# Kernel optimization log

Hardware: AMD Instinct MI355X
Metric: run time of the kernel (lower is better)

Reference implementation:

```python
import jax, jax.numpy as jnp
import numpy as np

D_MODEL = 1024
D_ATTN = 1024
BATCH = 4
SEQ = 2048


def setup_inputs() -> dict:
    key = jax.random.key(0)
    k_x, k_q, k_k, k_v = jax.random.split(key, 4)
    return {
        "x": jax.random.normal(k_x, (BATCH, SEQ, D_MODEL), dtype=jnp.float32),
        "Wq": jax.random.normal(k_q, (D_MODEL, D_ATTN), dtype=jnp.float32),
        "Wk": jax.random.normal(k_k, (D_MODEL, D_ATTN), dtype=jnp.float32),
        "Wv": jax.random.normal(k_v, (D_MODEL, D_ATTN), dtype=jnp.float32),
    }


def reference(x, Wq, Wk, Wv):
    # x: [B, S, D]; Wq/Wk/Wv: [D, Da]
    B, S, _ = x.shape
    Da = Wq.shape[1]
    Q = jnp.einsum("bsd,da->bsa", x, Wq)
    K = jnp.einsum("bsd,da->bsa", x, Wk)
    V = jnp.einsum("bsd,da->bsa", x, Wv)
    scores = jnp.einsum("bia,bja->bij", Q, K)  # [B, S, S]
    # Faithful to source: tril with diagonal=1 (allows attending one step ahead)
    i = jnp.arange(S)[:, None]
    j = jnp.arange(S)[None, :]
    allowed = j <= i + 1  # [S, S] bool
    scores = jnp.where(allowed[None, :, :], scores, -jnp.inf)
    scale = jnp.sqrt(jnp.asarray(Da, dtype=scores.dtype))
    attn = jax.nn.softmax(scores / scale, axis=-1)
    # dropout p=0 -> identity
    return jnp.einsum("bij,bja->bia", attn, V)
```

## Files before the change

kernel.cpp:

```cpp
#include <hip/hip_runtime.h>
#include <math.h>

#define BATCH 4
#define SEQ 2048
#define DM 1024
#define NTOK (BATCH * SEQ)
#define NE ((size_t)NTOK * DM)
#define WN ((size_t)DM * DM)

using s16x8 = __attribute__((ext_vector_type(8))) short;
using f32x4 = __attribute__((ext_vector_type(4))) float;

__device__ __forceinline__ unsigned short f2bf(float f) {
    unsigned u = __builtin_bit_cast(unsigned, f);
    u += 0x7FFFu + ((u >> 16) & 1u);
    return (unsigned short)(u >> 16);
}
__device__ __forceinline__ float bf2f(unsigned short h) {
    unsigned u = ((unsigned)h) << 16;
    return __builtin_bit_cast(float, u);
}

__device__ __forceinline__ f32x4 MFMA(s16x8 a, s16x8 b, f32x4 c) {
    return __builtin_amdgcn_mfma_f32_16x16x32_bf16(a, b, c, 0, 0, 0);
}

#define AS1 __attribute__((address_space(1)))
#define AS3 __attribute__((address_space(3)))
__device__ __forceinline__ void gll16(const void* g, void* l) {
    __builtin_amdgcn_global_load_lds((const AS1 void*)g, (AS3 void*)l, 16, 0, 0);
}

__device__ __forceinline__ s16x8 lds_frag(const short* base, int row, int g) {
    return *(const s16x8*)(base + row * 64 + ((g ^ (row & 7)) << 3));
}

__device__ __forceinline__ void stage_tile(const unsigned short* g0, size_t rs,
                                           short* lds, int tid) {
    int lane = tid & 63, w = tid >> 6;
    #pragma unroll
    for (int c = 0; c < 4; ++c) {
        int s = c * 256 + w * 64 + lane;
        int row = s >> 3, gg = s & 7;
        int graw = gg ^ (row & 7);
        gll16(g0 + (size_t)row * rs + graw * 8, lds + (size_t)s * 8);
    }
}

__global__ __launch_bounds__(256) void split_x(const float* __restrict__ x,
                                               unsigned short* __restrict__ xh,
                                               unsigned short* __restrict__ xl) {
    size_t n4 = NE / 4;
    for (size_t i = (size_t)blockIdx.x * 256 + threadIdx.x; i < n4;
         i += (size_t)gridDim.x * 256) {
        float4 v = ((const float4*)x)[i];
        ushort4 h, l;
        h.x = f2bf(v.x); l.x = f2bf(v.x - bf2f(h.x));
        h.y = f2bf(v.y); l.y = f2bf(v.y - bf2f(h.y));
        h.z = f2bf(v.z); l.z = f2bf(v.z - bf2f(h.z));
        h.w = f2bf(v.w); l.w = f2bf(v.w - bf2f(h.w));
        ((ushort4*)xh)[i] = h;
        ((ushort4*)xl)[i] = l;
    }
}

__global__ __launch_bounds__(256) void split_w(
    const float* __restrict__ Wq, const float* __restrict__ Wk,
    const float* __restrict__ Wv,
    unsigned short* __restrict__ Wqh, unsigned short* __restrict__ Wql,
    unsigned short* __restrict__ Wkh, unsigned short* __restrict__ Wkl,
    unsigned short* __restrict__ Wvt) {
    const int z = blockIdx.z;
    const int tid = threadIdx.x;
    if (z < 2) {
        const float* W = z ? Wk : Wq;
        unsigned short* oh = z ? Wkh : Wqh;
        unsigned short* ol = z ? Wkl : Wql;
        size_t n4 = WN / 4;
        size_t stride = (size_t)gridDim.x * gridDim.y * 256;
        for (size_t i = ((size_t)blockIdx.y * gridDim.x + blockIdx.x) * 256 + tid;
             i < n4; i += stride) {
            float4 v = ((const float4*)W)[i];
            ushort4 h, l;
            h.x = f2bf(v.x); l.x = f2bf(v.x - bf2f(h.x));
            h.y = f2bf(v.y); l.y = f2bf(v.y - bf2f(h.y));
            h.z = f2bf(v.z); l.z = f2bf(v.z - bf2f(h.z));
            h.w = f2bf(v.w); l.w = f2bf(v.w - bf2f(h.w));
            ((ushort4*)oh)[i] = h;
            ((ushort4*)ol)[i] = l;
        }
    } else {
        __shared__ float t[64][65];
        const int d0 = blockIdx.x * 64, n0 = blockIdx.y * 64;
        #pragma unroll
        for (int c = 0; c < 16; ++c) {
            int f = c * 256 + tid; int r = f >> 6, cc = f & 63;
            t[r][cc] = Wv[(size_t)(d0 + r) * DM + n0 + cc];
        }
        __syncthreads();
        #pragma unroll
        for (int c = 0; c < 16; ++c) {
            int f = c * 256 + tid; int r = f >> 6, cc = f & 63;
            Wvt[(size_t)(n0 + r) * DM + d0 + cc] = f2bf(t[cc][r]);
        }
    }
}

__global__ __launch_bounds__(256, 2) void gemm3_split(
    const unsigned short* __restrict__ Ah_, const unsigned short* __restrict__ Al_,
    const unsigned short* __restrict__ Bh_, const unsigned short* __restrict__ Bl_,
    unsigned short* __restrict__ Ch, unsigned short* __restrict__ Cl) {
    const int m0 = blockIdx.x * 128, n0 = blockIdx.y * 128;
    __shared__ short Ah[128 * 64], Al[128 * 64], Bh[128 * 64], Bl[128 * 64];
    const int tid = threadIdx.x, lane = tid & 63, w = tid >> 6;
    const int wr = w >> 1, wc = w & 1;

    f32x4 acc[4][4];
    #pragma unroll
    for (int i = 0; i < 4; ++i)
        #pragma unroll
        for (int j = 0; j < 4; ++j) acc[i][j] = (f32x4){0.f, 0.f, 0.f, 0.f};

    for (int k0 = 0; k0 < DM; k0 += 64) {
        stage_tile(Ah_ + (size_t)m0 * DM + k0, DM, Ah, tid);
        stage_tile(Al_ + (size_t)m0 * DM + k0, DM, Al, tid);
        stage_tile(Bh_ + (size_t)n0 * DM + k0, DM, Bh, tid);
        stage_tile(Bl_ + (size_t)n0 * DM + k0, DM, Bl, tid);
        __syncthreads();
        #pragma unroll
        for (int ks = 0; ks < 2; ++ks) {
            const int g = ks * 4 + (lane >> 4);
            s16x8 a_h[4], a_l[4], b_h[4], b_l[4];
            #pragma unroll
            for (int mi = 0; mi < 4; ++mi) {
                int r = wr * 64 + mi * 16 + (lane & 15);
                a_h[mi] = lds_frag(Ah, r, g);
                a_l[mi] = lds_frag(Al, r, g);
            }
            #pragma unroll
            for (int ni = 0; ni < 4; ++ni) {
                int r = wc * 64 + ni * 16 + (lane & 15);
                b_h[ni] = lds_frag(Bh, r, g);
                b_l[ni] = lds_frag(Bl, r, g);
            }
            #pragma unroll
            for (int mi = 0; mi < 4; ++mi)
                #pragma unroll
                for (int ni = 0; ni < 4; ++ni) {
                    acc[mi][ni] = MFMA(a_h[mi], b_h[ni], acc[mi][ni]);
                    acc[mi][ni] = MFMA(a_h[mi], b_l[ni], acc[mi][ni]);
                    acc[mi][ni] = MFMA(a_l[mi], b_h[ni], acc[mi][ni]);
                }
        }
        __syncthreads();
    }
    #pragma unroll
    for (int mi = 0; mi < 4; ++mi)
        #pragma unroll
        for (int ni = 0; ni < 4; ++ni)
            #pragma unroll
            for (int r = 0; r < 4; ++r) {
                int row = m0 + wr * 64 + mi * 16 + (lane >> 4) * 4 + r;
                int col = n0 + wc * 64 + ni * 16 + (lane & 15);
                float v = acc[mi][ni][r];
                unsigned short h = f2bf(v);
                size_t o = (size_t)row * DM + col;
                Ch[o] = h;
                Cl[o] = f2bf(v - bf2f(h));
            }
}

__global__ __launch_bounds__(256, 2) void vt_mfma(
    const unsigned short* __restrict__ Wvt, const unsigned short* __restrict__ xh,
    unsigned short* __restrict__ Vt) {
    const int m0 = blockIdx.x * 128;
    const int n0 = blockIdx.y * 128;
    __shared__ short Ah[128 * 64], Bh[128 * 64];
    const int tid = threadIdx.x, lane = tid & 63, w = tid >> 6;
    const int wr = w >> 1, wc = w & 1;

    f32x4 acc[4][4];
    #pragma unroll
    for (int i = 0; i < 4; ++i)
        #pragma unroll
        for (int j = 0; j < 4; ++j) acc[i][j] = (f32x4){0.f, 0.f, 0.f, 0.f};

    for (int k0 = 0; k0 < DM; k0 += 64) {
        stage_tile(Wvt + (size_t)m0 * DM + k0, DM, Ah, tid);
        stage_tile(xh + (size_t)n0 * DM + k0, DM, Bh, tid);
        __syncthreads();
        #pragma unroll
        for (int ks = 0; ks < 2; ++ks) {
            const int g = ks * 4 + (lane >> 4);
            s16x8 a_h[4], b_h[4];
            #pragma unroll
            for (int mi = 0; mi < 4; ++mi)
                a_h[mi] = lds_frag(Ah, wr * 64 + mi * 16 + (lane & 15), g);
            #pragma unroll
            for (int ni = 0; ni < 4; ++ni)
                b_h[ni] = lds_frag(Bh, wc * 64 + ni * 16 + (lane & 15), g);
            #pragma unroll
            for (int mi = 0; mi < 4; ++mi)
                #pragma unroll
                for (int ni = 0; ni < 4; ++ni)
                    acc[mi][ni] = MFMA(a_h[mi], b_h[ni], acc[mi][ni]);
        }
        __syncthreads();
    }
    #pragma unroll
    for (int mi = 0; mi < 4; ++mi)
        #pragma unroll
        for (int ni = 0; ni < 4; ++ni)
            #pragma unroll
            for (int r = 0; r < 4; ++r) {
                int row = m0 + wr * 64 + mi * 16 + (lane >> 4) * 4 + r;
                int col = n0 + wc * 64 + ni * 16 + (lane & 15);
                Vt[(size_t)row * NTOK + col] = f2bf(acc[mi][ni][r]);
            }
}

__global__ __launch_bounds__(256, 2) void scores_mfma(
    const unsigned short* __restrict__ Yh, const unsigned short* __restrict__ Yl,
    const unsigned short* __restrict__ xh, const unsigned short* __restrict__ xl,
    float* __restrict__ P) {
    const int jt = blockIdx.x, t = blockIdx.y, b = blockIdx.z;
    if (jt > t + 1) return;
    const int m0 = t * 128, n0 = jt * 128;
    const size_t qrow0 = (size_t)b * SEQ + m0;
    const size_t krow0 = (size_t)b * SEQ + n0;

    __shared__ short Ah[128 * 64], Al[128 * 64], Bh[128 * 64], Bl[128 * 64];
    const int tid = threadIdx.x, lane = tid & 63, w = tid >> 6;
    const int wr = w >> 1, wc = w & 1;

    f32x4 acc[4][4];
    #pragma unroll
    for (int i = 0; i < 4; ++i)
        #pragma unroll
        for (int j = 0; j < 4; ++j) acc[i][j] = (f32x4){0.f, 0.f, 0.f, 0.f};

    for (int k0 = 0; k0 < DM; k0 += 64) {
        stage_tile(Yh + qrow0 * DM + k0, DM, Ah, tid);
        stage_tile(Yl + qrow0 * DM + k0, DM, Al, tid);
        stage_tile(xh + krow0 * DM + k0, DM, Bh, tid);
        stage_tile(xl + krow0 * DM + k0, DM, Bl, tid);
        __syncthreads();
        #pragma unroll
        for (int ks = 0; ks < 2; ++ks) {
            const int g = ks * 4 + (lane >> 4);
            s16x8 a_h[4], a_l[4], b_h[4], b_l[4];
            #pragma unroll
            for (int mi = 0; mi < 4; ++mi) {
                int r = wr * 64 + mi * 16 + (lane & 15);
                a_h[mi] = lds_frag(Ah, r, g);
                a_l[mi] = lds_frag(Al, r, g);
            }
            #pragma unroll
            for (int ni = 0; ni < 4; ++ni) {
                int r = wc * 64 + ni * 16 + (lane & 15);
                b_h[ni] = lds_frag(Bh, r, g);
                b_l[ni] = lds_frag(Bl, r, g);
            }
            #pragma unroll
            for (int mi = 0; mi < 4; ++mi)
                #pragma unroll
                for (int ni = 0; ni < 4; ++ni) {
                    acc[mi][ni] = MFMA(a_h[mi], b_h[ni], acc[mi][ni]);
                    acc[mi][ni] = MFMA(a_h[mi], b_l[ni], acc[mi][ni]);
                    acc[mi][ni] = MFMA(a_l[mi], b_h[ni], acc[mi][ni]);
                }
        }
        __syncthreads();
    }
    const float scale = 1.0f / 32.0f;
    #pragma unroll
    for (int mi = 0; mi < 4; ++mi)
        #pragma unroll
        for (int ni = 0; ni < 4; ++ni)
            #pragma unroll
            for (int r = 0; r < 4; ++r) {
                int i = m0 + wr * 64 + mi * 16 + (lane >> 4) * 4 + r;
                int j = n0 + wc * 64 + ni * 16 + (lane & 15);
                float v = (j <= i + 1) ? acc[mi][ni][r] * scale : -INFINITY;
                P[((size_t)b * SEQ + i) * SEQ + j] = v;
            }
}

__global__ __launch_bounds__(256) void softmax_bf16(
    const float* __restrict__ P, unsigned short* __restrict__ P2) {
    const int row = blockIdx.x;
    const int b = row >> 11, i = row & (SEQ - 1);
    const int t = i >> 7;
    const int L = min(SEQ, (t + 2) * 128);
    const float* p = P + ((size_t)b * SEQ + i) * SEQ;
    unsigned short* q = P2 + ((size_t)b * SEQ + i) * SEQ;
    const int tid = threadIdx.x;
    __shared__ float red[4];

    float v[8];
    #pragma unroll
    for (int c = 0; c < 8; ++c) {
        int j = c * 256 + tid;
        v[c] = (j < L) ? p[j] : -INFINITY;
    }
    float m = -INFINITY;
    #pragma unroll
    for (int c = 0; c < 8; ++c) m = fmaxf(m, v[c]);
    #pragma unroll
    for (int o = 32; o > 0; o >>= 1) m = fmaxf(m, __shfl_xor(m, o));
    if ((tid & 63) == 0) red[tid >> 6] = m;
    __syncthreads();
    m = fmaxf(fmaxf(red[0], red[1]), fmaxf(red[2], red[3]));
    __syncthreads();

    float s = 0.f;
    #pragma unroll
    for (int c = 0; c < 8; ++c) { v[c] = __expf(v[c] - m); s += v[c]; }
    #pragma unroll
    for (int o = 32; o > 0; o >>= 1) s += __shfl_xor(s, o);
    if ((tid & 63) == 0) red[tid >> 6] = s;
    __syncthreads();
    s = red[0] + red[1] + red[2] + red[3];
    const float inv = 1.f / s;

    #pragma unroll
    for (int c = 0; c < 8; ++c) {
        int j = c * 256 + tid;
        if (j < L) q[j] = f2bf(v[c] * inv);
    }
}

__global__ __launch_bounds__(256, 2) void pv_mfma(
    const unsigned short* __restrict__ P2, const unsigned short* __restrict__ Vt,
    float* __restrict__ Out) {
    const int bx = blockIdx.x, t = blockIdx.y, b = blockIdx.z;
    const int m0 = t * 128, n0 = bx * 128;
    const int jlim = min(SEQ, (t + 2) * 128);

    __shared__ short Pa[128 * 64], Vb[128 * 64];
    const int tid = threadIdx.x, lane = tid & 63, w = tid >> 6;
    const int wr = w >> 1, wc = w & 1;

    f32x4 acc[4][4];
    #pragma unroll
    for (int i = 0; i < 4; ++i)
        #pragma unroll
        for (int j = 0; j < 4; ++j) acc[i][j] = (f32x4){0.f, 0.f, 0.f, 0.f};

    for (int k0 = 0; k0 < jlim; k0 += 64) {
        stage_tile(P2 + ((size_t)b * SEQ + m0) * SEQ + k0, SEQ, Pa, tid);
        stage_tile(Vt + (size_t)n0 * NTOK + (size_t)b * SEQ + k0, NTOK, Vb, tid);
        __syncthreads();
        #pragma unroll
        for (int ks = 0; ks < 2; ++ks) {
            const int g = ks * 4 + (lane >> 4);
            s16x8 a_h[4], b_h[4];
            #pragma unroll
            for (int mi = 0; mi < 4; ++mi)
                a_h[mi] = lds_frag(Pa, wr * 64 + mi * 16 + (lane & 15), g);
            #pragma unroll
            for (int ni = 0; ni < 4; ++ni)
                b_h[ni] = lds_frag(Vb, wc * 64 + ni * 16 + (lane & 15), g);
            #pragma unroll
            for (int mi = 0; mi < 4; ++mi)
                #pragma unroll
                for (int ni = 0; ni < 4; ++ni)
                    acc[mi][ni] = MFMA(a_h[mi], b_h[ni], acc[mi][ni]);
        }
        __syncthreads();
    }
    #pragma unroll
    for (int mi = 0; mi < 4; ++mi)
        #pragma unroll
        for (int ni = 0; ni < 4; ++ni)
            #pragma unroll
            for (int r = 0; r < 4; ++r) {
                int i = m0 + wr * 64 + mi * 16 + (lane >> 4) * 4 + r;
                int col = n0 + wc * 64 + ni * 16 + (lane & 15);
                Out[((size_t)b * SEQ + i) * DM + col] = acc[mi][ni][r];
            }
}

extern "C" void kernel_launch(void* const* d_in, const int* in_sizes, int n_in,
                              void* d_out, int out_size, void* d_ws, size_t ws_size,
                              hipStream_t stream) {
    const float* x  = (const float*)d_in[0];
    const float* Wq = (const float*)d_in[1];
    const float* Wk = (const float*)d_in[2];
    const float* Wv = (const float*)d_in[3];

    char* ws = (char*)d_ws;
    unsigned short* Vt = (unsigned short*)ws;
    unsigned short* xh = (unsigned short*)(ws + 2 * NE);
    unsigned short* xl = (unsigned short*)(ws + 4 * NE);
    float* P = (float*)(ws + 6 * NE);
    unsigned short* P2 = (unsigned short*)(ws + 2 * NE);
    unsigned short* Wqh = (unsigned short*)(ws + 6 * NE);
    unsigned short* Wql = Wqh + WN;
    unsigned short* Wkh = Wql + WN;
    unsigned short* Wkl = Wkh + WN;
    unsigned short* Mh  = Wkl + WN;
    unsigned short* Ml  = Mh + WN;
    unsigned short* Wvt = Ml + WN;
    unsigned short* Yh = (unsigned short*)d_out;
    unsigned short* Yl = Yh + NE;

    split_x<<<2048, 256, 0, stream>>>(x, xh, xl);
    {
        dim3 g(16, 16, 3);
        split_w<<<g, 256, 0, stream>>>(Wq, Wk, Wv, Wqh, Wql, Wkh, Wkl, Wvt);
    }
    {
        dim3 g(8, 8);
        gemm3_split<<<g, 256, 0, stream>>>(Wkh, Wkl, Wqh, Wql, Mh, Ml);
    }
    {
        dim3 g(NTOK / 128, DM / 128);
        gemm3_split<<<g, 256, 0, stream>>>(xh, xl, Mh, Ml, Yh, Yl);
    }
    {
        dim3 g(DM / 128, NTOK / 128);
        vt_mfma<<<g, 256, 0, stream>>>(Wvt, xh, Vt);
    }
    {
        dim3 g(16, 16, 4);
        scores_mfma<<<g, 256, 0, stream>>>(Yh, Yl, xh, xl, P);
    }
    softmax_bf16<<<BATCH * SEQ, 256, 0, stream>>>(P, P2);
    {
        dim3 g(DM / 128, 16, 4);
        pv_mfma<<<g, 256, 0, stream>>>(P2, Vt, (float*)d_out);
    }
}
```

Baseline: 324.4 us.

## Split-K the Wk·Wqᵀ GEMM, fuse it with the V projection, and remap block order

The small 1024x1024 M = Wk·Wqᵀ GEMM, which previously launched only 64 blocks, is split 8-way along K into fp32 slabs. It runs in one fused launch alongside the V-projection blocks, and a separate reduce kernel sums the slabs and splits the result into bf16 hi/lo. Scores and PV kernels also remap linear block IDs so that consecutive blocks are strided across 8 groups, likely to spread work across XCDs and improve cache locality. The cost is extra fp32 slab traffic and one added launch.

```diff
diff --git a/kernel.cpp b/kernel.cpp
--- a/kernel.cpp
+++ b/kernel.cpp
@@ -106,6 +106,132 @@
     }
 }
 
+__global__ __launch_bounds__(256, 2) void mvt_fused(
+    const unsigned short* __restrict__ Wkh_, const unsigned short* __restrict__ Wkl_,
+    const unsigned short* __restrict__ Wqh_, const unsigned short* __restrict__ Wql_,
+    float* __restrict__ Mslab,
+    const unsigned short* __restrict__ Wvt_, const unsigned short* __restrict__ xh_,
+    unsigned short* __restrict__ Vt) {
+    __shared__ short L[4 * 128 * 64];
+    short* Ah = L;            short* Al = L + 128 * 64;
+    short* Bh = L + 2 * 128 * 64; short* Bl = L + 3 * 128 * 64;
+    const int tid = threadIdx.x, lane = tid & 63, w = tid >> 6;
+    const int wr = w >> 1, wc = w & 1;
+    const int bid = blockIdx.x;
+
+    f32x4 acc[4][4];
+    #pragma unroll
+    for (int i = 0; i < 4; ++i)
+        #pragma unroll
+        for (int j = 0; j < 4; ++j) acc[i][j] = (f32x4){0.f, 0.f, 0.f, 0.f};
+
+    if (bid < 512) {
+        const int kz = bid >> 6, rem = bid & 63;
+        const int m0 = (rem & 7) * 128, n0 = (rem >> 3) * 128;
+        #pragma unroll
+        for (int kk = 0; kk < 2; ++kk) {
+            const int k0 = kz * 128 + kk * 64;
+            stage_tile(Wkh_ + (size_t)m0 * DM + k0, DM, Ah, tid);
+            stage_tile(Wkl_ + (size_t)m0 * DM + k0, DM, Al, tid);
+            stage_tile(Wqh_ + (size_t)n0 * DM + k0, DM, Bh, tid);
+            stage_tile(Wql_ + (size_t)n0 * DM + k0, DM, Bl, tid);
+            __syncthreads();
+            #pragma unroll
+            for (int ks = 0; ks < 2; ++ks) {
+                const int g = ks * 4 + (lane >> 4);
+                s16x8 a_h[4], a_l[4], b_h[4], b_l[4];
+                #pragma unroll
+                for (int mi = 0; mi < 4; ++mi) {
+                    int r = wr * 64 + mi * 16 + (lane & 15);
+                    a_h[mi] = lds_frag(Ah, r, g);
+                    a_l[mi] = lds_frag(Al, r, g);
+                }
+                #pragma unroll
+                for (int ni = 0; ni < 4; ++ni) {
+                    int r = wc * 64 + ni * 16 + (lane & 15);
+                    b_h[ni] = lds_frag(Bh, r, g);
+                    b_l[ni] = lds_frag(Bl, r, g);
+                }
+                #pragma unroll
+                for (int mi = 0; mi < 4; ++mi)
+                    #pragma unroll
+                    for (int ni = 0; ni < 4; ++ni) {
+                        acc[mi][ni] = MFMA(a_h[mi], b_h[ni], acc[mi][ni]);
+                        acc[mi][ni] = MFMA(a_h[mi], b_l[ni], acc[mi][ni]);
+                        acc[mi][ni] = MFMA(a_l[mi], b_h[ni], acc[mi][ni]);
+                    }
+            }
+            __syncthreads();
+        }
+        float* out = Mslab + (size_t)kz * WN;
+        #pragma unroll
+        for (int mi = 0; mi < 4; ++mi)
+            #pragma unroll
+            for (int ni = 0; ni < 4; ++ni)
+                #pragma unroll
+                for (int r = 0; r < 4; ++r) {
+                    int row = m0 + wr * 64 + mi * 16 + (lane >> 4) * 4 + r;
+                    int col = n0 + wc * 64 + ni * 16 + (lane & 15);
+                    out[(size_t)row * DM + col] = acc[mi][ni][r];
+                }
+    } else {
+        const int id2 = bid - 512;
+        const int m0 = (id2 & 7) * 128;
+        const int n0 = (id2 >> 3) * 128;
+        for (int k0 = 0; k0 < DM; k0 += 64) {
+            stage_tile(Wvt_ + (size_t)m0 * DM + k0, DM, Ah, tid);
+            stage_tile(xh_ + (size_t)n0 * DM + k0, DM, Bh, tid);
+            __syncthreads();
+            #pragma unroll
+            for (int ks = 0; ks < 2; ++ks) {
+                const int g = ks * 4 + (lane >> 4);
+                s16x8 a_h[4], b_h[4];
+                #pragma unroll
+                for (int mi = 0; mi < 4; ++mi)
+                    a_h[mi] = lds_frag(Ah, wr * 64 + mi * 16 + (lane & 15), g);
+                #pragma unroll
+                for (int ni = 0; ni < 4; ++ni)
+                    b_h[ni] = lds_frag(Bh, wc * 64 + ni * 16 + (lane & 15), g);
+                #pragma unroll
+                for (int mi = 0; mi < 4; ++mi)
+                    #pragma unroll
+                    for (int ni = 0; ni < 4; ++ni)
+                        acc[mi][ni] = MFMA(a_h[mi], b_h[ni], acc[mi][ni]);
+            }
+            __syncthreads();
+        }
+        #pragma unroll
+        for (int mi = 0; mi < 4; ++mi)
+            #pragma unroll
+            for (int ni = 0; ni < 4; ++ni)
+                #pragma unroll
+                for (int r = 0; r < 4; ++r) {
+                    int row = m0 + wr * 64 + mi * 16 + (lane >> 4) * 4 + r;
+                    int col = n0 + wc * 64 + ni * 16 + (lane & 15);
+                    Vt[(size_t)row * NTOK + col] = f2bf(acc[mi][ni][r]);
+                }
+    }
+}
+
+__global__ __launch_bounds__(256) void mreduce(
+    const float* __restrict__ Mslab,
+    unsigned short* __restrict__ Mh, unsigned short* __restrict__ Ml) {
+    size_t i = (size_t)blockIdx.x * 256 + threadIdx.x;
+    float4 s = ((const float4*)Mslab)[i];
+    #pragma unroll
+    for (int r = 1; r < 8; ++r) {
+        float4 v = ((const float4*)(Mslab + (size_t)r * WN))[i];
+        s.x += v.x; s.y += v.y; s.z += v.z; s.w += v.w;
+    }
+    ushort4 h, l;
+    h.x = f2bf(s.x); l.x = f2bf(s.x - bf2f(h.x));
+    h.y = f2bf(s.y); l.y = f2bf(s.y - bf2f(h.y));
+    h.z = f2bf(s.z); l.z = f2bf(s.z - bf2f(h.z));
+    h.w = f2bf(s.w); l.w = f2bf(s.w - bf2f(h.w));
+    ((ushort4*)Mh)[i] = h;
+    ((ushort4*)Ml)[i] = l;
+}
+
 __global__ __launch_bounds__(256, 2) void gemm3_split(
     const unsigned short* __restrict__ Ah_, const unsigned short* __restrict__ Al_,
     const unsigned short* __restrict__ Bh_, const unsigned short* __restrict__ Bl_,
@@ -170,60 +296,13 @@
             }
 }
 
-__global__ __launch_bounds__(256, 2) void vt_mfma(
-    const unsigned short* __restrict__ Wvt, const unsigned short* __restrict__ xh,
-    unsigned short* __restrict__ Vt) {
-    const int m0 = blockIdx.x * 128;
-    const int n0 = blockIdx.y * 128;
-    __shared__ short Ah[128 * 64], Bh[128 * 64];
-    const int tid = threadIdx.x, lane = tid & 63, w = tid >> 6;
-    const int wr = w >> 1, wc = w & 1;
-
-    f32x4 acc[4][4];
-    #pragma unroll
-    for (int i = 0; i < 4; ++i)
-        #pragma unroll
-        for (int j = 0; j < 4; ++j) acc[i][j] = (f32x4){0.f, 0.f, 0.f, 0.f};
-
-    for (int k0 = 0; k0 < DM; k0 += 64) {
-        stage_tile(Wvt + (size_t)m0 * DM + k0, DM, Ah, tid);
-        stage_tile(xh + (size_t)n0 * DM + k0, DM, Bh, tid);
-        __syncthreads();
-        #pragma unroll
-        for (int ks = 0; ks < 2; ++ks) {
-            const int g = ks * 4 + (lane >> 4);
-            s16x8 a_h[4], b_h[4];
-            #pragma unroll
-            for (int mi = 0; mi < 4; ++mi)
-                a_h[mi] = lds_frag(Ah, wr * 64 + mi * 16 + (lane & 15), g);
-            #pragma unroll
-            for (int ni = 0; ni < 4; ++ni)
-                b_h[ni] = lds_frag(Bh, wc * 64 + ni * 16 + (lane & 15), g);
-            #pragma unroll
-            for (int mi = 0; mi < 4; ++mi)
-                #pragma unroll
-                for (int ni = 0; ni < 4; ++ni)
-                    acc[mi][ni] = MFMA(a_h[mi], b_h[ni], acc[mi][ni]);
-        }
-        __syncthreads();
-    }
-    #pragma unroll
-    for (int mi = 0; mi < 4; ++mi)
-        #pragma unroll
-        for (int ni = 0; ni < 4; ++ni)
-            #pragma unroll
-            for (int r = 0; r < 4; ++r) {
-                int row = m0 + wr * 64 + mi * 16 + (lane >> 4) * 4 + r;
-                int col = n0 + wc * 64 + ni * 16 + (lane & 15);
-                Vt[(size_t)row * NTOK + col] = f2bf(acc[mi][ni][r]);
-            }
-}
-
 __global__ __launch_bounds__(256, 2) void scores_mfma(
     const unsigned short* __restrict__ Yh, const unsigned short* __restrict__ Yl,
     const unsigned short* __restrict__ xh, const unsigned short* __restrict__ xl,
     float* __restrict__ P) {
-    const int jt = blockIdx.x, t = blockIdx.y, b = blockIdx.z;
+    const int lin = (blockIdx.z * gridDim.y + blockIdx.y) * gridDim.x + blockIdx.x;
+    const int logical = (lin & 7) * 128 + (lin >> 3);
+    const int jt = logical & 15, t = (logical >> 4) & 15, b = logical >> 8;
     if (jt > t + 1) return;
     const int m0 = t * 128, n0 = jt * 128;
     const size_t qrow0 = (size_t)b * SEQ + m0;
@@ -333,7 +412,9 @@
 __global__ __launch_bounds__(256, 2) void pv_mfma(
     const unsigned short* __restrict__ P2, const unsigned short* __restrict__ Vt,
     float* __restrict__ Out) {
-    const int bx = blockIdx.x, t = blockIdx.y, b = blockIdx.z;
+    const int lin = (blockIdx.z * gridDim.y + blockIdx.y) * gridDim.x + blockIdx.x;
+    const int logical = (lin & 7) * 64 + (lin >> 3);
+    const int bx = logical & 7, t = (logical >> 3) & 15, b = logical >> 7;
     const int m0 = t * 128, n0 = bx * 128;
     const int jlim = min(SEQ, (t + 2) * 128);
 
@@ -402,6 +483,7 @@
     unsigned short* Mh  = Wkl + WN;
     unsigned short* Ml  = Mh + WN;
     unsigned short* Wvt = Ml + WN;
+    float* Mslab = (float*)(ws + 6 * NE + 7 * WN * 2);
     unsigned short* Yh = (unsigned short*)d_out;
     unsigned short* Yl = Yh + NE;
 
@@ -410,25 +492,19 @@
         dim3 g(16, 16, 3);
         split_w<<<g, 256, 0, stream>>>(Wq, Wk, Wv, Wqh, Wql, Wkh, Wkl, Wvt);
     }
-    {
-        dim3 g(8, 8);
-        gemm3_split<<<g, 256, 0, stream>>>(Wkh, Wkl, Wqh, Wql, Mh, Ml);
-    }
+    mvt_fused<<<1024, 256, 0, stream>>>(Wkh, Wkl, Wqh, Wql, Mslab, Wvt, xh, Vt);
+    mreduce<<<1024, 256, 0, stream>>>(Mslab, Mh, Ml);
     {
         dim3 g(NTOK / 128, DM / 128);
         gemm3_split<<<g, 256, 0, stream>>>(xh, xl, Mh, Ml, Yh, Yl);
     }
     {
-        dim3 g(DM / 128, NTOK / 128);
-        vt_mfma<<<g, 256, 0, stream>>>(Wvt, xh, Vt);
-    }
-    {
         dim3 g(16, 16, 4);
         scores_mfma<<<g, 256, 0, stream>>>(Yh, Yl, xh, xl, P);
     }
     softmax_bf16<<<BATCH * SEQ, 256, 0, stream>>>(P, P2);
     {
-        dim3 g(DM / 128, 16, 4);
+        dim3 g(8, 16, 4);
         pv_mfma<<<g, 256, 0, stream>>>(P2, Vt, (float*)d_out);
     }
 }
```

Measured after the change: 297.2 us. 8.4% less time.
